# Performance work log

Measured on AMD Instinct MI355X. Metric: run time of the kernel, lower is better.

Reference implementation:

```python
import jax, jax.numpy as jnp
import numpy as np

MODEL_DIM = 1024
NUM_HEADS = 16
HEAD_DIM = MODEL_DIM // NUM_HEADS
ROPE_BASE = 10000.0


def apply_rope(x):
    # x: [B, H, S, D] -- rotate-half RoPE convention
    S, D = x.shape[-2], x.shape[-1]
    inv_freq = 1.0 / (ROPE_BASE ** (jnp.arange(0, D, 2, dtype=jnp.float32) / D))  # [D/2]
    t = jnp.arange(S, dtype=jnp.float32)
    freqs = t[:, None] * inv_freq[None, :]                  # [S, D/2]
    cos = jnp.concatenate([jnp.cos(freqs), jnp.cos(freqs)], axis=-1)  # [S, D]
    sin = jnp.concatenate([jnp.sin(freqs), jnp.sin(freqs)], axis=-1)
    x1, x2 = x[..., : D // 2], x[..., D // 2 :]
    rot = jnp.concatenate([-x2, x1], axis=-1)
    return x * cos + rot * sin


def setup_inputs() -> dict:
    key = jax.random.key(0)
    k1, k2, k3 = jax.random.split(key, 3)
    B, S, Dm = 4, 2048, MODEL_DIM
    std = 1.0 / np.sqrt(Dm)
    x = jax.random.normal(k1, (B, S, Dm), dtype=jnp.float32)
    w_qkv = jax.random.normal(k2, (Dm, 3 * Dm), dtype=jnp.float32) * std
    b_qkv = jnp.zeros((3 * Dm,), dtype=jnp.float32)
    w_out = jax.random.normal(k3, (Dm, Dm), dtype=jnp.float32) * std
    b_out = jnp.zeros((Dm,), dtype=jnp.float32)
    return {"x": x, "w_qkv": w_qkv, "b_qkv": b_qkv, "w_out": w_out, "b_out": b_out}


def reference(x, w_qkv, b_qkv, w_out, b_out):
    B, S, Dm = x.shape
    H, Dh = NUM_HEADS, HEAD_DIM
    scale = Dh ** -0.5
    qkv = x @ w_qkv + b_qkv                                  # [B, S, 3*Dm]
    qkv = qkv.reshape(B, S, 3, H, Dh).transpose(2, 0, 3, 1, 4)  # [3, B, H, S, Dh]
    q, k, v = qkv[0], qkv[1], qkv[2]
    q = apply_rope(q)
    k = apply_rope(k)
    scores = jnp.einsum("bhqd,bhkd->bhqk", q, k) * scale      # [B, H, S, S]
    causal = jnp.tril(jnp.ones((S, S), dtype=bool))
    scores = jnp.where(causal[None, None], scores, -jnp.inf)
    attn = jax.nn.softmax(scores, axis=-1)
    out = jnp.einsum("bhqk,bhkd->bhqd", attn, v)              # [B, H, S, Dh]
    out = out.transpose(0, 2, 1, 3).reshape(B, S, Dm)
    out = out @ w_out + b_out
    return out, attn
```

## Files before the change

### kernel.cpp

```cpp
#include <hip/hip_runtime.h>
#include <hip/hip_bf16.h>
#include <stdint.h>

typedef unsigned short u16;
typedef __attribute__((ext_vector_type(4))) float f32x4;
typedef __attribute__((ext_vector_type(8))) short s16x8;

#define SEQ 2048
#define NB 4
#define DM 1024
#define NHD 16
#define DH 64

__device__ __forceinline__ u16 f2bf(float f) {
  union { float f; uint32_t u; } v; v.f = f;
  return (u16)((v.u + 0x7FFFu + ((v.u >> 16) & 1u)) >> 16);
}
__device__ __forceinline__ float bf2f(u16 u) {
  union { uint32_t u; float f; } v; v.u = ((uint32_t)u) << 16;
  return v.f;
}
__device__ __forceinline__ void gload16(const u16* g, u16* l) {
  __builtin_amdgcn_global_load_lds((const __attribute__((address_space(1))) void*)g,
                                   (__attribute__((address_space(3))) void*)l, 16, 0, 0);
}

__device__ __forceinline__ void stage64x64_swz(const u16* gbase, long gstride,
                                               u16* lds, int tid) {
  int l = tid & 63, w = tid >> 6;
  int rsub = l >> 3;
  int srcElem = ((l & 7) ^ rsub) * 8;
  #pragma unroll
  for (int p = 0; p < 2; ++p) {
    int row0 = w * 16 + p * 8;
    gload16(gbase + (long)(row0 + rsub) * gstride + srcElem, lds + row0 * 64);
  }
}
__device__ __forceinline__ s16x8 frag_swz(const u16* lds, int row, int cb) {
  return *(const s16x8*)&lds[row * 64 + (cb ^ ((row & 7) << 3))];
}

__global__ __launch_bounds__(256) void k_cvt(const float* __restrict__ in,
                                             u16* __restrict__ out, int n4) {
  int idx = blockIdx.x * 256 + threadIdx.x;
  int stride = gridDim.x * 256;
  for (; idx < n4; idx += stride) {
    float4 v = ((const float4*)in)[idx];
    ushort4 o;
    o.x = f2bf(v.x); o.y = f2bf(v.y); o.z = f2bf(v.z); o.w = f2bf(v.w);
    ((ushort4*)out)[idx] = o;
  }
}

__global__ __launch_bounds__(256) void k_tpose(const float* __restrict__ in,
                                               u16* __restrict__ out, int R, int C) {
  __shared__ u16 tile[64][65];
  int c0 = blockIdx.x * 64, r0 = blockIdx.y * 64;
  int tx = threadIdx.x & 63, ty = threadIdx.x >> 6;
  #pragma unroll
  for (int rr = ty; rr < 64; rr += 4)
    tile[rr][tx] = f2bf(in[(long)(r0 + rr) * C + c0 + tx]);
  __syncthreads();
  #pragma unroll
  for (int cc = ty; cc < 64; cc += 4)
    out[(long)(c0 + cc) * R + r0 + tx] = tile[tx][cc];
}

template<int OUT_BF16>
__global__ __launch_bounds__(256) void k_gemm(const u16* __restrict__ A,
                                              const u16* __restrict__ Bt_g,
                                              const float* __restrict__ bias,
                                              void* __restrict__ Cout,
                                              int M, int N, int K) {
  __shared__ u16 As[128 * 32];
  __shared__ u16 Bs[128 * 32];
  int tid = threadIdx.x, lane = tid & 63, wave = tid >> 6;
  int wm = (wave >> 1) * 64, wn = (wave & 1) * 64;
  long m0 = (long)blockIdx.y * 128, n0 = (long)blockIdx.x * 128;
  int lrow = lane & 15, lk8 = (lane >> 4) * 8;
  int srow = wave * 16 + (lane >> 2);
  int scol = (lane & 3) * 8;
  const u16* Ag = &A[(m0 + srow) * (long)K + scol];
  const u16* Bg = &Bt_g[(n0 + srow) * (long)K + scol];
  u16* lA0 = &As[(wave * 16) * 32];
  u16* lA1 = &As[(64 + wave * 16) * 32];
  u16* lB0 = &Bs[(wave * 16) * 32];
  u16* lB1 = &Bs[(64 + wave * 16) * 32];
  f32x4 acc[4][4] = {};
  for (int k0 = 0; k0 < K; k0 += 32) {
    __syncthreads();
    gload16(Ag + k0, lA0);
    gload16(Ag + 64L * K + k0, lA1);
    gload16(Bg + k0, lB0);
    gload16(Bg + 64L * K + k0, lB1);
    __syncthreads();
    s16x8 af[4], bfr[4];
    #pragma unroll
    for (int t = 0; t < 4; ++t) af[t]  = *(const s16x8*)&As[(wm + t * 16 + lrow) * 32 + lk8];
    #pragma unroll
    for (int t = 0; t < 4; ++t) bfr[t] = *(const s16x8*)&Bs[(wn + t * 16 + lrow) * 32 + lk8];
    #pragma unroll
    for (int i = 0; i < 4; ++i)
      #pragma unroll
      for (int j = 0; j < 4; ++j)
        acc[i][j] = __builtin_amdgcn_mfma_f32_16x16x32_bf16(af[i], bfr[j], acc[i][j], 0, 0, 0);
  }
  int crow = (lane >> 4) * 4, ccol = lane & 15;
  #pragma unroll
  for (int i = 0; i < 4; ++i)
  #pragma unroll
  for (int j = 0; j < 4; ++j) {
    long col = n0 + wn + j * 16 + ccol;
    float bv = bias ? bias[col] : 0.f;
    #pragma unroll
    for (int r = 0; r < 4; ++r) {
      long row = m0 + wm + i * 16 + crow + r;
      float v = acc[i][j][r] + bv;
      if (OUT_BF16) ((u16*)Cout)[row * N + col] = f2bf(v);
      else          ((float*)Cout)[row * N + col] = v;
    }
  }
}

__global__ __launch_bounds__(256) void k_rope(const u16* __restrict__ qkv,
                                              u16* __restrict__ Qr,
                                              u16* __restrict__ Kr) {
  int t = blockIdx.x * 256 + threadIdx.x;
  int i = t & 31;
  int h = (t >> 5) & 15;
  int s = (t >> 9) & 2047;
  int b = t >> 20;
  long row = ((long)(b * SEQ + s)) * 3072 + h * 64;
  float q1 = bf2f(qkv[row + i]),        q2 = bf2f(qkv[row + i + 32]);
  float k1 = bf2f(qkv[row + 1024 + i]), k2 = bf2f(qkv[row + 1024 + i + 32]);
  float fq = exp2f(-(float)i * 0.4152410118609203f);
  float ang = (float)s * fq;
  float c = cosf(ang), sn = sinf(ang);
  long ob = ((long)((b * NHD + h) * SEQ + s)) * 64;
  Qr[ob + i]      = f2bf((q1 * c - q2 * sn) * 0.125f);
  Qr[ob + i + 32] = f2bf((q2 * c + q1 * sn) * 0.125f);
  Kr[ob + i]      = f2bf(k1 * c - k2 * sn);
  Kr[ob + i + 32] = f2bf(k2 * c + k1 * sn);
}

__global__ __launch_bounds__(256) void k_vt(const u16* __restrict__ qkv,
                                            u16* __restrict__ VtG) {
  __shared__ u16 t[64][65];
  int jt = blockIdx.x, bh = blockIdx.y;
  int b = bh >> 4, h = bh & 15;
  int tid = threadIdx.x;
  int r = tid >> 3, c8 = (tid & 7) * 8;
  long base = ((long)(b * SEQ + jt * 64)) * 3072 + 2048 + h * 64;
  #pragma unroll
  for (int half = 0; half < 2; ++half) {
    s16x8 v = *(const s16x8*)&qkv[base + (long)(r + half * 32) * 3072 + c8];
    #pragma unroll
    for (int j = 0; j < 8; ++j) t[r + half * 32][c8 + j] = (u16)v[j];
  }
  __syncthreads();
  long ob = ((long)bh * 32 + jt) * 4096;
  int d = tid >> 3, r8 = (tid & 7) * 8;
  #pragma unroll
  for (int half = 0; half < 2; ++half) {
    s16x8 o;
    #pragma unroll
    for (int j = 0; j < 8; ++j) o[j] = (short)t[r8 + j][d + half * 32];
    *(s16x8*)&VtG[ob + (long)(d + half * 32) * 64 + r8] = o;
  }
}

__global__ __launch_bounds__(256) void k_attn(const u16* __restrict__ Qr,
                                              const u16* __restrict__ Kr,
                                              const u16* __restrict__ VtG,
                                              float* __restrict__ attn,
                                              u16* __restrict__ ctx) {
  constexpr int LP = 72;
  __shared__ u16 Ks[64 * 64];
  __shared__ u16 Vs[64 * 64];
  __shared__ u16 Ps[4][16 * LP];
  int tid = threadIdx.x, lane = tid & 63, wave = tid >> 6;
  int bh = blockIdx.y;
  int q0 = blockIdx.x * 64;
  int qw0 = q0 + wave * 16;
  int lrow = lane & 15, lg = lane >> 4, lk8 = (lane >> 4) * 8;
  const u16* Qb = Qr + (long)bh * SEQ * 64;
  const u16* Kb = Kr + (long)bh * SEQ * 64;
  const u16* Vtb = VtG + (long)bh * 32 * 4096;
  float* attn_bh = attn + (long)bh * SEQ * SEQ;

  s16x8 qf0 = *(const s16x8*)&Qb[(long)(qw0 + lrow) * 64 + lk8];
  s16x8 qf1 = *(const s16x8*)&Qb[(long)(qw0 + lrow) * 64 + 32 + lk8];

  int njt = blockIdx.x + 1;

  float suml[4] = {0.f, 0.f, 0.f, 0.f};
  for (int jt = 0; jt < njt; ++jt) {
    __syncthreads();
    stage64x64_swz(Kb + (long)jt * 64 * 64, 64, Ks, tid);
    __syncthreads();
    int ctmax = (jt < njt - 1) ? 3 : wave;
    long k0 = (long)jt * 64;
    for (int ct = 0; ct <= ctmax; ++ct) {
      int row = ct * 16 + lrow;
      s16x8 kf0 = frag_swz(Ks, row, lk8);
      s16x8 kf1 = frag_swz(Ks, row, 32 + lk8);
      f32x4 sa = {0.f, 0.f, 0.f, 0.f};
      sa = __builtin_amdgcn_mfma_f32_16x16x32_bf16(qf0, kf0, sa, 0, 0, 0);
      sa = __builtin_amdgcn_mfma_f32_16x16x32_bf16(qf1, kf1, sa, 0, 0, 0);
      bool diag = (jt == njt - 1) && (ct == wave);
      int gcol = (int)k0 + ct * 16 + lrow;
      #pragma unroll
      for (int r = 0; r < 4; ++r) {
        int grow = qw0 + lg * 4 + r;
        float e = (!diag || gcol <= grow) ? __expf(sa[r]) : 0.f;
        suml[r] += e;
      }
    }
  }
  #pragma unroll
  for (int r = 0; r < 4; ++r) {
    float v = suml[r];
    v += __shfl_xor(v, 1, 16);
    v += __shfl_xor(v, 2, 16);
    v += __shfl_xor(v, 4, 16);
    v += __shfl_xor(v, 8, 16);
    suml[r] = 1.0f / v;
  }

  f32x4 oacc[4] = {};
  u16* ps = &Ps[wave][0];
  for (int jt = 0; jt < njt; ++jt) {
    __syncthreads();
    stage64x64_swz(Kb + (long)jt * 64 * 64, 64, Ks, tid);
    stage64x64_swz(Vtb + jt * 4096, 64, Vs, tid);
    __syncthreads();
    int ctmax = (jt < njt - 1) ? 3 : wave;
    long k0 = (long)jt * 64;
    #pragma unroll
    for (int ct = 0; ct < 4; ++ct) {
      if (ct <= ctmax) {
        int row = ct * 16 + lrow;
        s16x8 kf0 = frag_swz(Ks, row, lk8);
        s16x8 kf1 = frag_swz(Ks, row, 32 + lk8);
        f32x4 sa = {0.f, 0.f, 0.f, 0.f};
        sa = __builtin_amdgcn_mfma_f32_16x16x32_bf16(qf0, kf0, sa, 0, 0, 0);
        sa = __builtin_amdgcn_mfma_f32_16x16x32_bf16(qf1, kf1, sa, 0, 0, 0);
        bool diag = (jt == njt - 1) && (ct == wave);
        int gcol = (int)k0 + ct * 16 + lrow;
        #pragma unroll
        for (int r = 0; r < 4; ++r) {
          int grow = qw0 + lg * 4 + r;
          float e = (!diag || gcol <= grow) ? __expf(sa[r]) : 0.f;
          ps[(lg * 4 + r) * LP + ct * 16 + lrow] = f2bf(e * suml[r]);
        }
      } else {
        #pragma unroll
        for (int r = 0; r < 4; ++r)
          ps[(lg * 4 + r) * LP + ct * 16 + lrow] = 0;
      }
    }
    s16x8 pf0 = *(const s16x8*)&ps[lrow * LP + lk8];
    s16x8 pf1 = *(const s16x8*)&ps[lrow * LP + 32 + lk8];
    #pragma unroll
    for (int dt = 0; dt < 4; ++dt) {
      int row = dt * 16 + lrow;
      s16x8 vf0 = frag_swz(Vs, row, lk8);
      s16x8 vf1 = frag_swz(Vs, row, 32 + lk8);
      oacc[dt] = __builtin_amdgcn_mfma_f32_16x16x32_bf16(pf0, vf0, oacc[dt], 0, 0, 0);
      oacc[dt] = __builtin_amdgcn_mfma_f32_16x16x32_bf16(pf1, vf1, oacc[dt], 0, 0, 0);
    }
    #pragma unroll
    for (int it = 0; it < 4; ++it) {
      int prow = it * 4 + (lane >> 4);
      int c4 = lane & 15;
      ushort4 pv = *(const ushort4*)&ps[prow * LP + c4 * 4];
      f32x4 o;
      o.x = bf2f(pv.x); o.y = bf2f(pv.y); o.z = bf2f(pv.z); o.w = bf2f(pv.w);
      __builtin_nontemporal_store(o,
          (f32x4*)&attn_bh[(long)(qw0 + prow) * SEQ + k0 + c4 * 4]);
    }
  }

  {
    int cstart = q0 + 64;
    int zc4 = (SEQ - cstart) >> 2;
    f32x4 z = {0.f, 0.f, 0.f, 0.f};
    for (int row = 0; row < 64; ++row) {
      f32x4* dst = (f32x4*)&attn_bh[(long)(q0 + row) * SEQ + cstart];
      for (int cc = tid; cc < zc4; cc += 256)
        __builtin_nontemporal_store(z, &dst[cc]);
    }
  }

  int b = bh >> 4, h = bh & 15;
  #pragma unroll
  for (int dt = 0; dt < 4; ++dt)
  #pragma unroll
  for (int r = 0; r < 4; ++r) {
    long grow = qw0 + lg * 4 + r;
    long col = h * 64 + dt * 16 + lrow;
    ctx[((long)b * SEQ + grow) * DM + col] = f2bf(oacc[dt][r]);
  }
}

extern "C" void kernel_launch(void* const* d_in, const int* in_sizes, int n_in,
                              void* d_out, int out_size, void* d_ws, size_t ws_size,
                              hipStream_t stream) {
  const float* x     = (const float*)d_in[0];
  const float* w_qkv = (const float*)d_in[1];
  const float* b_qkv = (const float*)d_in[2];
  const float* w_out = (const float*)d_in[3];
  const float* b_out = (const float*)d_in[4];
  float* outp = (float*)d_out;
  float* attn = outp + (long)NB * SEQ * DM;

  char* ws = (char*)d_ws;
  u16* Qr  = (u16*)(ws);
  u16* Kr  = (u16*)(ws + 16777216L);
  u16* VtG = (u16*)(ws + 33554432L);
  u16* ctx = (u16*)(ws + 50331648L);
  u16* WoT = (u16*)(ws + 67108864L);

  u16* qkvb = (u16*)attn;
  u16* Xb   = (u16*)((char*)attn + 50331648L);
  u16* WqT  = (u16*)((char*)attn + 67108864L);

  k_cvt<<<1024, 256, 0, stream>>>(x, Xb, (NB * SEQ * DM) / 4);
  k_tpose<<<dim3(3 * DM / 64, DM / 64), 256, 0, stream>>>(w_qkv, WqT, DM, 3 * DM);
  k_tpose<<<dim3(DM / 64, DM / 64), 256, 0, stream>>>(w_out, WoT, DM, DM);

  k_gemm<1><<<dim3(3 * DM / 128, NB * SEQ / 128), 256, 0, stream>>>(
      Xb, WqT, b_qkv, qkvb, NB * SEQ, 3 * DM, DM);

  k_rope<<<(NB * SEQ * NHD * 32) / 256, 256, 0, stream>>>(qkvb, Qr, Kr);
  k_vt<<<dim3(SEQ / 64, NB * NHD), 256, 0, stream>>>(qkvb, VtG);

  k_attn<<<dim3(SEQ / 64, NB * NHD), 256, 0, stream>>>(Qr, Kr, VtG, attn, ctx);

  k_gemm<0><<<dim3(DM / 128, NB * SEQ / 128), 256, 0, stream>>>(
      ctx, WoT, b_out, outp, NB * SEQ, DM, DM);
}
```

Measured before the change: 434.9 us.

## Double GEMM K-tile to 64 and reorder attention blocks heaviest-first with XCD grouping

The GEMM now stages a 128x64 K-slice per barrier pair instead of 128x32, halving the number of syncs and global-to-LDS rounds per output tile at the cost of doubling LDS use. The attention kernel moves to a 1D grid whose block index is remapped so the longest causal query tiles are scheduled first. Consecutive block IDs (presumably round-robined across the 8 XCDs) map to eight different heads, so the same heads stay on one XCD and can share its K/V in L2. This targets load imbalance from causal work and cross-die cache misses.

```diff
diff --git a/kernel.cpp b/kernel.cpp
--- a/kernel.cpp
+++ b/kernel.cpp
@@ -72,38 +72,40 @@
                                               const float* __restrict__ bias,
                                               void* __restrict__ Cout,
                                               int M, int N, int K) {
-  __shared__ u16 As[128 * 32];
-  __shared__ u16 Bs[128 * 32];
+  __shared__ u16 As[128 * 64];
+  __shared__ u16 Bs[128 * 64];
   int tid = threadIdx.x, lane = tid & 63, wave = tid >> 6;
   int wm = (wave >> 1) * 64, wn = (wave & 1) * 64;
   long m0 = (long)blockIdx.y * 128, n0 = (long)blockIdx.x * 128;
   int lrow = lane & 15, lk8 = (lane >> 4) * 8;
-  int srow = wave * 16 + (lane >> 2);
-  int scol = (lane & 3) * 8;
+  int srow = wave * 8 + (lane >> 3);
+  int scol = (lane & 7) * 8;
   const u16* Ag = &A[(m0 + srow) * (long)K + scol];
   const u16* Bg = &Bt_g[(n0 + srow) * (long)K + scol];
-  u16* lA0 = &As[(wave * 16) * 32];
-  u16* lA1 = &As[(64 + wave * 16) * 32];
-  u16* lB0 = &Bs[(wave * 16) * 32];
-  u16* lB1 = &Bs[(64 + wave * 16) * 32];
   f32x4 acc[4][4] = {};
-  for (int k0 = 0; k0 < K; k0 += 32) {
-    __syncthreads();
-    gload16(Ag + k0, lA0);
-    gload16(Ag + 64L * K + k0, lA1);
-    gload16(Bg + k0, lB0);
-    gload16(Bg + 64L * K + k0, lB1);
-    __syncthreads();
-    s16x8 af[4], bfr[4];
-    #pragma unroll
-    for (int t = 0; t < 4; ++t) af[t]  = *(const s16x8*)&As[(wm + t * 16 + lrow) * 32 + lk8];
-    #pragma unroll
-    for (int t = 0; t < 4; ++t) bfr[t] = *(const s16x8*)&Bs[(wn + t * 16 + lrow) * 32 + lk8];
-    #pragma unroll
-    for (int i = 0; i < 4; ++i)
+  for (int k0 = 0; k0 < K; k0 += 64) {
+    __syncthreads();
+    #pragma unroll
+    for (int p = 0; p < 4; ++p) {
+      gload16(Ag + (long)p * 32 * K + k0, &As[(p * 32 + wave * 8) * 64]);
+      gload16(Bg + (long)p * 32 * K + k0, &Bs[(p * 32 + wave * 8) * 64]);
+    }
+    __syncthreads();
+    #pragma unroll
+    for (int h = 0; h < 2; ++h) {
+      s16x8 af[4], bfr[4];
       #pragma unroll
-      for (int j = 0; j < 4; ++j)
-        acc[i][j] = __builtin_amdgcn_mfma_f32_16x16x32_bf16(af[i], bfr[j], acc[i][j], 0, 0, 0);
+      for (int t = 0; t < 4; ++t)
+        af[t]  = *(const s16x8*)&As[(wm + t * 16 + lrow) * 64 + h * 32 + lk8];
+      #pragma unroll
+      for (int t = 0; t < 4; ++t)
+        bfr[t] = *(const s16x8*)&Bs[(wn + t * 16 + lrow) * 64 + h * 32 + lk8];
+      #pragma unroll
+      for (int i = 0; i < 4; ++i)
+        #pragma unroll
+        for (int j = 0; j < 4; ++j)
+          acc[i][j] = __builtin_amdgcn_mfma_f32_16x16x32_bf16(af[i], bfr[j], acc[i][j], 0, 0, 0);
+    }
   }
   int crow = (lane >> 4) * 4, ccol = lane & 15;
   #pragma unroll
@@ -179,8 +181,11 @@
   __shared__ u16 Vs[64 * 64];
   __shared__ u16 Ps[4][16 * LP];
   int tid = threadIdx.x, lane = tid & 63, wave = tid >> 6;
-  int bh = blockIdx.y;
-  int q0 = blockIdx.x * 64;
+  int wgid = blockIdx.x;
+  int c = wgid & 7, t7 = wgid >> 3;
+  int bh = c * 8 + (t7 >> 5);
+  int qb = 31 - (t7 & 31);
+  int q0 = qb * 64;
   int qw0 = q0 + wave * 16;
   int lrow = lane & 15, lg = lane >> 4, lk8 = (lane >> 4) * 8;
   const u16* Qb = Qr + (long)bh * SEQ * 64;
@@ -191,7 +196,7 @@
   s16x8 qf0 = *(const s16x8*)&Qb[(long)(qw0 + lrow) * 64 + lk8];
   s16x8 qf1 = *(const s16x8*)&Qb[(long)(qw0 + lrow) * 64 + 32 + lk8];
 
-  int njt = blockIdx.x + 1;
+  int njt = qb + 1;
 
   float suml[4] = {0.f, 0.f, 0.f, 0.f};
   for (int jt = 0; jt < njt; ++jt) {
@@ -335,7 +340,7 @@
   k_rope<<<(NB * SEQ * NHD * 32) / 256, 256, 0, stream>>>(qkvb, Qr, Kr);
   k_vt<<<dim3(SEQ / 64, NB * NHD), 256, 0, stream>>>(qkvb, VtG);
 
-  k_attn<<<dim3(SEQ / 64, NB * NHD), 256, 0, stream>>>(Qr, Kr, VtG, attn, ctx);
+  k_attn<<<2048, 256, 0, stream>>>(Qr, Kr, VtG, attn, ctx);
 
   k_gemm<0><<<dim3(DM / 128, NB * SEQ / 128), 256, 0, stream>>>(
       ctx, WoT, b_out, outp, NB * SEQ, DM, DM);
```

Result: faster. 398.6 us (-8.4%).
